# Kernel optimization log

Measured on AMD Instinct MI355X. Metric: run time of the kernel, lower is better.

The kernel has to match this reference:

```python
import jax, jax.numpy as jnp
import numpy as np
from jax import lax

B, T, I, H, O = 256, 2048, 50, 116, 50


def setup_inputs() -> dict:
    key = jax.random.key(0)
    ks = jax.random.split(key, 7)
    k = 1.0 / np.sqrt(H)  # torch default uniform init bound for nn.RNN / nn.Linear
    u = lambda kk, shp: jax.random.uniform(kk, shp, jnp.float32, -k, k)
    return {
        "x": jax.random.normal(ks[0], (B, T, I), jnp.float32),
        "W_ih": u(ks[1], (H, I)),
        "b_ih": u(ks[2], (H,)),
        "W_hh": u(ks[3], (H, H)),
        "b_hh": u(ks[4], (H,)),
        "W_fc": u(ks[5], (O, H)),
        "b_fc": u(ks[6], (O,)),
    }


def reference(x, W_ih, b_ih, W_hh, b_hh, W_fc, b_fc):
    # Precompute input contribution for all timesteps: [B, T, H]
    xp = jnp.einsum("bti,hi->bth", x, W_ih) + b_ih + b_hh

    def step(h, xt):
        # h: [B, H], xt: [B, H]; Elman ReLU cell
        h_new = jax.nn.relu(xt + h @ W_hh.T)
        return h_new, h_new

    h0 = jnp.zeros((x.shape[0], W_hh.shape[0]), x.dtype)
    _, hs = lax.scan(step, h0, jnp.swapaxes(xp, 0, 1))  # hs: [T, B, H]
    out = jnp.swapaxes(hs, 0, 1)  # [B, T, H]
    out = jax.nn.relu(out)  # trailing ReLU (no-op after ReLU cell, kept for fidelity)
    return out @ W_fc.T + b_fc  # [B, T, O]
```

## Files before the change

### kernel.cpp

```cpp
#include <hip/hip_runtime.h>


namespace {
constexpr int kB = 256;
constexpr int kT = 2048;
constexpr int kI = 50;
constexpr int kH = 116;
constexpr int kO = 50;
}

struct Smem {
  alignas(16) float h[2][144];
  alignas(16) float xp[2][128];
  alignas(16) float xr[4][52];
};

__device__ __forceinline__ void sync_lds() {
  __asm__ __volatile__("s_waitcnt lgkmcnt(0)\n\ts_barrier" ::: "memory");
}

__device__ __forceinline__ float qadd1(float v) {
  return v + __int_as_float(__builtin_amdgcn_update_dpp(
                 0, __float_as_int(v), 0xB1, 0xF, 0xF, true));
}
__device__ __forceinline__ float qadd2(float v) {
  return v + __int_as_float(__builtin_amdgcn_update_dpp(
                 0, __float_as_int(v), 0x4E, 0xF, 0xF, true));
}

__device__ __forceinline__ void h_step(Smem& sm, int pw, int pr,
                                       const float (&w)[4][32], int k,
                                       int rowk, int hwr, bool wvalid) {
  const float xpv = sm.xp[pw][rowk];
  const float4* hp4 = (const float4*)sm.h[pr];
  float4 hc[8];
#pragma unroll
  for (int i = 0; i < 8; ++i) hc[i] = hp4[9 * k + i];
  float res = 0.f;
#pragma unroll
  for (int p = 0; p < 4; ++p) {
    float s0 = 0.f, s1 = 0.f, s2 = 0.f, s3 = 0.f;
#pragma unroll
    for (int i = 0; i < 8; ++i) {
      const float4 v = hc[i];
      s0 = fmaf(w[p][4 * i + 0], v.x, s0);
      s1 = fmaf(w[p][4 * i + 1], v.y, s1);
      s2 = fmaf(w[p][4 * i + 2], v.z, s2);
      s3 = fmaf(w[p][4 * i + 3], v.w, s3);
    }
    float c = (s0 + s1) + (s2 + s3);
    c = qadd2(qadd1(c));
    res = (k == p) ? c : res;
  }
  res += xpv;
  res = res > 0.f ? res : 0.f;
  if (wvalid) sm.h[pw][hwr] = res;
}

__device__ __forceinline__ void fc_step(Smem& sm, int slot,
                                        const float (&w)[4][32], int k,
                                        int rowk, float bfc,
                                        float* __restrict__ ob, size_t ubase) {
  const float4* hp4 = (const float4*)sm.h[slot];
  float4 hc[8];
#pragma unroll
  for (int i = 0; i < 8; ++i) hc[i] = hp4[9 * k + i];
  float res = 0.f;
#pragma unroll
  for (int p = 0; p < 4; ++p) {
    float s0 = 0.f, s1 = 0.f, s2 = 0.f, s3 = 0.f;
#pragma unroll
    for (int i = 0; i < 8; ++i) {
      const float4 v = hc[i];
      s0 = fmaf(w[p][4 * i + 0], v.x, s0);
      s1 = fmaf(w[p][4 * i + 1], v.y, s1);
      s2 = fmaf(w[p][4 * i + 2], v.z, s2);
      s3 = fmaf(w[p][4 * i + 3], v.w, s3);
    }
    float c = (s0 + s1) + (s2 + s3);
    c = qadd2(qadd1(c));
    res = (k == p) ? c : res;
  }
  res += bfc;
  if (rowk < kO) ob[ubase + rowk] = res;
}

__device__ __forceinline__ void xp_step(Smem& sm, int xs, int xpp,
                                        const float (&wi0)[kI],
                                        const float (&wi1)[kI],
                                        float bias0, float bias1, int ln) {
  const float4* xq = (const float4*)sm.xr[xs];
  float s00 = 0.f, s01 = 0.f, s02 = 0.f, s03 = 0.f;
  float s10 = 0.f, s11 = 0.f, s12 = 0.f, s13 = 0.f;
#pragma unroll
  for (int i = 0; i < 12; ++i) {
    float4 v = xq[i];
    s00 = fmaf(wi0[4 * i + 0], v.x, s00);
    s01 = fmaf(wi0[4 * i + 1], v.y, s01);
    s02 = fmaf(wi0[4 * i + 2], v.z, s02);
    s03 = fmaf(wi0[4 * i + 3], v.w, s03);
    s10 = fmaf(wi1[4 * i + 0], v.x, s10);
    s11 = fmaf(wi1[4 * i + 1], v.y, s11);
    s12 = fmaf(wi1[4 * i + 2], v.z, s12);
    s13 = fmaf(wi1[4 * i + 3], v.w, s13);
  }
  float2 vt = ((const float2*)sm.xr[xs])[24];
  s00 = fmaf(wi0[48], vt.x, s00);
  s01 = fmaf(wi0[49], vt.y, s01);
  s10 = fmaf(wi1[48], vt.x, s10);
  s11 = fmaf(wi1[49], vt.y, s11);
  sm.xp[xpp][ln] = bias0 + ((s00 + s01) + (s02 + s03));
  if (ln < kH - 64) sm.xp[xpp][ln + 64] = bias1 + ((s10 + s11) + (s12 + s13));
}

__launch_bounds__(256, 1)
__global__ void rnn_fused(const float* __restrict__ x,
                          const float* __restrict__ W_ih,
                          const float* __restrict__ b_ih,
                          const float* __restrict__ W_hh,
                          const float* __restrict__ b_hh,
                          const float* __restrict__ W_fc,
                          const float* __restrict__ b_fc,
                          float* __restrict__ out) {
  __shared__ Smem sm;
  const int tid = threadIdx.x;
  const int wv = tid >> 6;
  const int ln = tid & 63;
  const int b = blockIdx.x;
  const float* xb = x + (size_t)b * (kT * kI);
  float* ob = out + (size_t)b * (kT * kO);

  float w[4][32];
  float wi0[kI], wi1[kI];
  float bias0 = 0.f, bias1 = 0.f, bfc = 0.f;
  float xr0 = 0.f, xr1 = 0.f, xr2 = 0.f, xr3 = 0.f;

  const int k = ln & 3;
  const int rl = ln >> 2;
  int rowk = 0, hwr = 0;
  bool wvalid = false;

  if (wv < 2) {
    const int rbase = 58 * wv;
    rowk = rbase + rl + 16 * k;
    wvalid = (rl + 16 * k) < 58;
    hwr = 36 * (rowk >> 5) + (rowk & 31);
#pragma unroll
    for (int p = 0; p < 4; ++p) {
      const int rloc = rl + 16 * p;
      const bool vr = rloc < 58;
      const size_t r = rbase + (vr ? rloc : 0);
#pragma unroll
      for (int j = 0; j < 32; ++j) {
        const int col = 32 * k + j;
        w[p][j] = (vr && col < kH) ? W_hh[r * kH + col] : 0.f;
      }
    }
  } else if (wv == 2) {
    rowk = rl + 16 * k;
#pragma unroll
    for (int p = 0; p < 4; ++p) {
      const int rloc = rl + 16 * p;
      const bool vr = rloc < kO;
      const size_t r = vr ? rloc : 0;
#pragma unroll
      for (int j = 0; j < 32; ++j) {
        const int col = 32 * k + j;
        w[p][j] = (vr && col < kH) ? W_fc[r * kH + col] : 0.f;
      }
    }
    bfc = (rowk < kO) ? b_fc[rowk] : 0.f;
  } else {
    {
      const float2* wr = (const float2*)(W_ih + ln * kI);
#pragma unroll
      for (int i = 0; i < kI / 2; ++i) {
        float2 v = wr[i]; wi0[2 * i] = v.x; wi0[2 * i + 1] = v.y;
      }
      bias0 = b_ih[ln] + b_hh[ln];
    }
    if (ln < kH - 64) {
      const float2* wr = (const float2*)(W_ih + (ln + 64) * kI);
#pragma unroll
      for (int i = 0; i < kI / 2; ++i) {
        float2 v = wr[i]; wi1[2 * i] = v.x; wi1[2 * i + 1] = v.y;
      }
      bias1 = b_ih[ln + 64] + b_hh[ln + 64];
    } else {
#pragma unroll
      for (int i = 0; i < kI; ++i) wi1[i] = 0.f;
    }
    if (ln < kI) {
      sm.xr[0][ln] = xb[0 * kI + ln];
      sm.xr[1][ln] = xb[1 * kI + ln];
      xr2 = xb[2 * kI + ln];
      xr3 = xb[3 * kI + ln];
      xr0 = xb[4 * kI + ln];
      xr1 = xb[5 * kI + ln];
    }
  }
  if (tid < 144) { sm.h[0][tid] = 0.f; sm.h[1][tid] = 0.f; }
  sync_lds();

  if (wv == 3) xp_step(sm, 0, 0, wi0, wi1, bias0, bias1, ln);
  sync_lds();

#define RNN_STEP(T_, XRV)                                                   \
  {                                                                         \
    const int t = (T_);                                                     \
    const int pw = t & 1, pr = (t + 1) & 1;                                 \
    if (wv < 2) {                                                           \
      h_step(sm, pw, pr, w, k, rowk, hwr, wvalid);                          \
    } else if (wv == 2) {                                                   \
      if (t > 0) fc_step(sm, pr, w, k, rowk, bfc, ob, (size_t)(t - 1) * kO);\
    } else {                                                                \
      xp_step(sm, (t + 1) & 3, (t + 1) & 1, wi0, wi1, bias0, bias1, ln);    \
      if (ln < kI) {                                                        \
        sm.xr[(t + 2) & 3][ln] = (XRV);                                     \
        int tf = t + 6; tf = tf < kT ? tf : kT - 1;                         \
        (XRV) = xb[(size_t)tf * kI + ln];                                   \
      }                                                                     \
    }                                                                       \
    sync_lds();                                                             \
  }

  for (int t0 = 0; t0 < kT; t0 += 4) {
    RNN_STEP(t0 + 0, xr2)
    RNN_STEP(t0 + 1, xr3)
    RNN_STEP(t0 + 2, xr0)
    RNN_STEP(t0 + 3, xr1)
  }
#undef RNN_STEP

  if (wv == 2) fc_step(sm, (kT - 1) & 1, w, k, rowk, bfc, ob,
                       (size_t)(kT - 1) * kO);
}

extern "C" void kernel_launch(void* const* d_in, const int* in_sizes, int n_in,
                              void* d_out, int out_size, void* d_ws, size_t ws_size,
                              hipStream_t stream) {
  (void)in_sizes; (void)n_in; (void)d_ws; (void)ws_size; (void)out_size;
  const float* x    = (const float*)d_in[0];
  const float* W_ih = (const float*)d_in[1];
  const float* b_ih = (const float*)d_in[2];
  const float* W_hh = (const float*)d_in[3];
  const float* b_hh = (const float*)d_in[4];
  const float* W_fc = (const float*)d_in[5];
  const float* b_fc = (const float*)d_in[6];
  float* out = (float*)d_out;
  rnn_fused<<<dim3(kB), dim3(256), 0, stream>>>(x, W_ih, b_ih, W_hh, b_hh,
                                                W_fc, b_fc, out);
}
```

Measured before the change: 1.209 ms.

## Replace per-step block barriers with LDS flag handshake and 8-step superstep pipeline

The two recurrence waves now sync only with each other through LDS flags, spinning on the partner wave's progress counter each timestep instead of taking a full workgroup barrier. The xp producer and fc consumer waves run in 8-step supersteps against deeper ring buffers (16 slots), so a block barrier is needed only once per superstep. The recurrence waves get raised scheduling priority. This aims to remove barrier latency from the serial critical path, but it relies on LDS ordering between waves without explicit waitcnt fences and adds spin-wait overhead.

```diff
diff --git a/kernel.cpp b/kernel.cpp
--- a/kernel.cpp
+++ b/kernel.cpp
@@ -7,16 +7,25 @@
 constexpr int kI = 50;
 constexpr int kH = 116;
 constexpr int kO = 50;
+constexpr int kSS = 8;
+constexpr int kHD = 16;
+constexpr int kXPD = 16;
 }
 
 struct Smem {
-  alignas(16) float h[2][144];
-  alignas(16) float xp[2][128];
+  alignas(16) float h[kHD][144];
+  alignas(16) float xp[kXPD][128];
   alignas(16) float xr[4][52];
+  int flags[2];
 };
 
 __device__ __forceinline__ void sync_lds() {
   __asm__ __volatile__("s_waitcnt lgkmcnt(0)\n\ts_barrier" ::: "memory");
+}
+
+__device__ __forceinline__ void wait_flag(const volatile int* f, int want) {
+  while (__builtin_amdgcn_readfirstlane(*f) < want) {}
+  __asm__ __volatile__("" ::: "memory");
 }
 
 __device__ __forceinline__ float qadd1(float v) {
@@ -28,11 +37,10 @@
                  0, __float_as_int(v), 0x4E, 0xF, 0xF, true));
 }
 
-__device__ __forceinline__ void h_step(Smem& sm, int pw, int pr,
-                                       const float (&w)[4][32], int k,
-                                       int rowk, int hwr, bool wvalid) {
-  const float xpv = sm.xp[pw][rowk];
-  const float4* hp4 = (const float4*)sm.h[pr];
+__device__ __forceinline__ void h_step(Smem& sm, int t, const float (&w)[4][32],
+                                       int k, int rowk, int hwr, bool wvalid) {
+  const float xpv = sm.xp[t & (kXPD - 1)][rowk];
+  const float4* hp4 = (const float4*)sm.h[(t + kHD - 1) & (kHD - 1)];
   float4 hc[8];
 #pragma unroll
   for (int i = 0; i < 8; ++i) hc[i] = hp4[9 * k + i];
@@ -54,14 +62,13 @@
   }
   res += xpv;
   res = res > 0.f ? res : 0.f;
-  if (wvalid) sm.h[pw][hwr] = res;
-}
-
-__device__ __forceinline__ void fc_step(Smem& sm, int slot,
-                                        const float (&w)[4][32], int k,
-                                        int rowk, float bfc,
-                                        float* __restrict__ ob, size_t ubase) {
-  const float4* hp4 = (const float4*)sm.h[slot];
+  if (wvalid) sm.h[t & (kHD - 1)][hwr] = res;
+}
+
+__device__ __forceinline__ void fc_step(Smem& sm, int u, const float (&w)[4][32],
+                                        int k, int rowk, float bfc,
+                                        float* __restrict__ ob) {
+  const float4* hp4 = (const float4*)sm.h[u & (kHD - 1)];
   float4 hc[8];
 #pragma unroll
   for (int i = 0; i < 8; ++i) hc[i] = hp4[9 * k + i];
@@ -82,10 +89,10 @@
     res = (k == p) ? c : res;
   }
   res += bfc;
-  if (rowk < kO) ob[ubase + rowk] = res;
-}
-
-__device__ __forceinline__ void xp_step(Smem& sm, int xs, int xpp,
+  if (rowk < kO) ob[(size_t)u * kO + rowk] = res;
+}
+
+__device__ __forceinline__ void xp_step(Smem& sm, int xs, int slot,
                                         const float (&wi0)[kI],
                                         const float (&wi1)[kI],
                                         float bias0, float bias1, int ln) {
@@ -109,8 +116,8 @@
   s01 = fmaf(wi0[49], vt.y, s01);
   s10 = fmaf(wi1[48], vt.x, s10);
   s11 = fmaf(wi1[49], vt.y, s11);
-  sm.xp[xpp][ln] = bias0 + ((s00 + s01) + (s02 + s03));
-  if (ln < kH - 64) sm.xp[xpp][ln + 64] = bias1 + ((s10 + s11) + (s12 + s13));
+  sm.xp[slot][ln] = bias0 + ((s00 + s01) + (s02 + s03));
+  if (ln < kH - 64) sm.xp[slot][ln + 64] = bias1 + ((s10 + s11) + (s12 + s13));
 }
 
 __launch_bounds__(256, 1)
@@ -133,7 +140,7 @@
   float w[4][32];
   float wi0[kI], wi1[kI];
   float bias0 = 0.f, bias1 = 0.f, bfc = 0.f;
-  float xr0 = 0.f, xr1 = 0.f, xr2 = 0.f, xr3 = 0.f;
+  float xrv[4] = {0.f, 0.f, 0.f, 0.f};
 
   const int k = ln & 3;
   const int rl = ln >> 2;
@@ -193,47 +200,76 @@
     if (ln < kI) {
       sm.xr[0][ln] = xb[0 * kI + ln];
       sm.xr[1][ln] = xb[1 * kI + ln];
-      xr2 = xb[2 * kI + ln];
-      xr3 = xb[3 * kI + ln];
-      xr0 = xb[4 * kI + ln];
-      xr1 = xb[5 * kI + ln];
-    }
-  }
-  if (tid < 144) { sm.h[0][tid] = 0.f; sm.h[1][tid] = 0.f; }
+      xrv[2] = xb[2 * kI + ln];
+      xrv[3] = xb[3 * kI + ln];
+      xrv[0] = xb[4 * kI + ln];
+      xrv[1] = xb[5 * kI + ln];
+    }
+  }
+  if (tid < 144) sm.h[kHD - 1][tid] = 0.f;
+  if (tid == 0) { sm.flags[0] = -1; sm.flags[1] = -1; }
   sync_lds();
 
-  if (wv == 3) xp_step(sm, 0, 0, wi0, wi1, bias0, bias1, ln);
+  if (wv < 2) __builtin_amdgcn_s_setprio(1);
+
+  if (wv == 3) {
+#pragma unroll
+    for (int j = 0; j < kSS; ++j) {
+      xp_step(sm, j & 3, j & (kXPD - 1), wi0, wi1, bias0, bias1, ln);
+      if (ln < kI) {
+        sm.xr[(j + 2) & 3][ln] = xrv[(j + 2) & 3];
+        const int tf = j + 6;
+        xrv[(j + 2) & 3] = xb[(size_t)tf * kI + ln];
+      }
+    }
+  }
   sync_lds();
 
-#define RNN_STEP(T_, XRV)                                                   \
-  {                                                                         \
-    const int t = (T_);                                                     \
-    const int pw = t & 1, pr = (t + 1) & 1;                                 \
-    if (wv < 2) {                                                           \
-      h_step(sm, pw, pr, w, k, rowk, hwr, wvalid);                          \
-    } else if (wv == 2) {                                                   \
-      if (t > 0) fc_step(sm, pr, w, k, rowk, bfc, ob, (size_t)(t - 1) * kO);\
-    } else {                                                                \
-      xp_step(sm, (t + 1) & 3, (t + 1) & 1, wi0, wi1, bias0, bias1, ln);    \
-      if (ln < kI) {                                                        \
-        sm.xr[(t + 2) & 3][ln] = (XRV);                                     \
-        int tf = t + 6; tf = tf < kT ? tf : kT - 1;                         \
-        (XRV) = xb[(size_t)tf * kI + ln];                                   \
-      }                                                                     \
-    }                                                                       \
-    sync_lds();                                                             \
-  }
-
-  for (int t0 = 0; t0 < kT; t0 += 4) {
-    RNN_STEP(t0 + 0, xr2)
-    RNN_STEP(t0 + 1, xr3)
-    RNN_STEP(t0 + 2, xr0)
-    RNN_STEP(t0 + 3, xr1)
-  }
-#undef RNN_STEP
-
-  if (wv == 2) fc_step(sm, (kT - 1) & 1, w, k, rowk, bfc, ob,
-                       (size_t)(kT - 1) * kO);
+  volatile int* my = (volatile int*)&sm.flags[wv & 1];
+  const volatile int* oth = (const volatile int*)&sm.flags[1 - (wv & 1)];
+
+#pragma unroll 1
+  for (int s = 0; s < kT / kSS; ++s) {
+    if (wv < 2) {
+      const int t0 = kSS * s;
+#pragma unroll
+      for (int j = 0; j < kSS; ++j) {
+        const int t = t0 + j;
+        if (j > 0) wait_flag(oth, t - 1);
+        h_step(sm, t, w, k, rowk, hwr, wvalid);
+        __asm__ __volatile__("" ::: "memory");
+        if (ln == 0) *my = t;
+      }
+    } else if (wv == 2) {
+      if (s > 0) {
+        const int u0 = kSS * (s - 1);
+#pragma unroll
+        for (int j = 0; j < kSS; ++j)
+          fc_step(sm, u0 + j, w, k, rowk, bfc, ob);
+      }
+    } else {
+      if (s < kT / kSS - 1) {
+        const int tau0 = kSS * s + kSS;
+#pragma unroll
+        for (int j = 0; j < kSS; ++j) {
+          const int tau = tau0 + j;
+          xp_step(sm, j & 3, tau & (kXPD - 1), wi0, wi1, bias0, bias1, ln);
+          if (ln < kI) {
+            sm.xr[(j + 2) & 3][ln] = xrv[(j + 2) & 3];
+            int tf = tau + 6; tf = tf < kT ? tf : kT - 1;
+            xrv[(j + 2) & 3] = xb[(size_t)tf * kI + ln];
+          }
+        }
+      }
+    }
+    sync_lds();
+  }
+
+  if (wv == 2) {
+#pragma unroll
+    for (int j = 0; j < kSS; ++j)
+      fc_step(sm, kT - kSS + j, w, k, rowk, bfc, ob);
+  }
 }
 
 extern "C" void kernel_launch(void* const* d_in, const int* in_sizes, int n_in,
```

Measured after the change: 1.056 ms. 1.14x faster.
